# Kernel optimization log

Hardware: AMD Instinct MI355X
Metric: run time of the kernel (lower is better)

The kernel has to match this reference:

```python
import jax, jax.numpy as jnp
import numpy as np

NUM_HEADS = 16
HEAD_DIM = 64  # d_out // num_heads = 1024 // 16


def setup_inputs() -> dict:
    key = jax.random.key(0)
    ks = jax.random.split(key, 9)
    B, S, D = 2, 2048, 1024
    scale = 0.02
    return {
        "x": jax.random.normal(ks[0], (B, S, D), jnp.float32),
        "Wq": jax.random.normal(ks[1], (D, D), jnp.float32) * scale,
        "bq": jax.random.normal(ks[2], (D,), jnp.float32) * scale,
        "Wk": jax.random.normal(ks[3], (D, D), jnp.float32) * scale,
        "bk": jax.random.normal(ks[4], (D,), jnp.float32) * scale,
        "Wv": jax.random.normal(ks[5], (D, D), jnp.float32) * scale,
        "bv": jax.random.normal(ks[6], (D,), jnp.float32) * scale,
        "Wo": jax.random.normal(ks[7], (D, D), jnp.float32) * scale,
        "bo": jax.random.normal(ks[8], (D,), jnp.float32) * scale,
    }


def reference(x, Wq, bq, Wk, bk, Wv, bv, Wo, bo):
    B, S, D = x.shape
    H, Dh = NUM_HEADS, HEAD_DIM
    # QKV projections (torch Linear: x @ W.T + b; here W stored as [d_in, d_out])
    q = (x @ Wq + bq).reshape(B, S, H, Dh).transpose(0, 2, 1, 3)  # [B,H,S,Dh]
    k = (x @ Wk + bk).reshape(B, S, H, Dh).transpose(0, 2, 1, 3)
    v = (x @ Wv + bv).reshape(B, S, H, Dh).transpose(0, 2, 1, 3)
    scores = jnp.einsum("bhqd,bhkd->bhqk", q, k)
    # causal mask applied before scaling (as in source; -inf unaffected by scale)
    causal = jnp.tril(jnp.ones((S, S), dtype=bool))
    scores = jnp.where(causal, scores, -jnp.inf) / jnp.sqrt(jnp.float32(Dh))
    attn = jax.nn.softmax(scores, axis=-1)  # dropout=0.0 (eval)
    ctx = jnp.einsum("bhqk,bhkd->bhqd", attn, v)  # [B,H,S,Dh]
    ctx = ctx.transpose(0, 2, 1, 3).reshape(B, S, D)
    return ctx @ Wo + bo
```

## Files before the change

### kernel.cpp

```cpp
#include <hip/hip_runtime.h>
#include <math.h>


#define H_  16
#define DH_ 64
#define D_  1024
#define S_  2048
#define B_  2

typedef __attribute__((ext_vector_type(8))) short short8;
typedef __attribute__((ext_vector_type(4))) float f32x4;

#define QSCALE 0.18033688011112042f
#define DEFER_THR 11.5416f

__device__ __forceinline__ unsigned short f2bf(float f) {
    union { float f; unsigned int u; } v; v.f = f;
    unsigned int r = (v.u + 0x7fffu + ((v.u >> 16) & 1u)) >> 16;
    return (unsigned short)r;
}

__device__ __forceinline__ unsigned cvt_pk_bf16(float lo, float hi) {
    unsigned r;
    asm("v_cvt_pk_bf16_f32 %0, %1, %2" : "=v"(r) : "v"(lo), "v"(hi));
    return r;
}

__device__ __forceinline__ float fast_exp2(float x) {
#if __has_builtin(__builtin_amdgcn_exp2f)
    return __builtin_amdgcn_exp2f(x);
#else
    return exp2f(x);
#endif
}

__device__ __forceinline__ void gload_lds16(const void* g, void* l) {
    __builtin_amdgcn_global_load_lds(
        (const __attribute__((address_space(1))) void*)g,
        (__attribute__((address_space(3))) void*)l, 16, 0, 0);
}

#define SYNC_VM0() asm volatile("s_waitcnt vmcnt(0)\n\ts_barrier" ::: "memory")

__global__ __launch_bounds__(256) void cvt_x_k(const float* __restrict__ x,
                                               unsigned short* __restrict__ xb)
{
    int i = (blockIdx.x * 256 + threadIdx.x) * 8;
    float4 a = *(const float4*)&x[i];
    float4 b = *(const float4*)&x[i + 4];
    uint4 o;
    o.x = f2bf(a.x) | ((unsigned)f2bf(a.y) << 16);
    o.y = f2bf(a.z) | ((unsigned)f2bf(a.w) << 16);
    o.z = f2bf(b.x) | ((unsigned)f2bf(b.y) << 16);
    o.w = f2bf(b.z) | ((unsigned)f2bf(b.w) << 16);
    *(uint4*)&xb[i] = o;
}

__global__ __launch_bounds__(256) void tr_w_k(
    const float* __restrict__ W0, const float* __restrict__ W1,
    const float* __restrict__ W2, const float* __restrict__ W3,
    unsigned short* __restrict__ wt)
{
    const float* W = W0;
    if (blockIdx.z == 1) W = W1; else if (blockIdx.z == 2) W = W2;
    else if (blockIdx.z == 3) W = W3;
    unsigned short* out = wt + (size_t)blockIdx.z * 1048576;

    __shared__ float t[64][65];
    const int k0 = blockIdx.x * 64, n0 = blockIdx.y * 64;
    const int r = threadIdx.x >> 4, c4 = (threadIdx.x & 15) * 4;

    #pragma unroll
    for (int p = 0; p < 4; ++p) {
        float4 v = *(const float4*)&W[(size_t)(k0 + r + 16 * p) * D_ + n0 + c4];
        t[r + 16 * p][c4 + 0] = v.x; t[r + 16 * p][c4 + 1] = v.y;
        t[r + 16 * p][c4 + 2] = v.z; t[r + 16 * p][c4 + 3] = v.w;
    }
    __syncthreads();
    #pragma unroll
    for (int p = 0; p < 4; ++p) {
        int nn = r + 16 * p;
        uint2 o;
        o.x = f2bf(t[c4 + 0][nn]) | ((unsigned)f2bf(t[c4 + 1][nn]) << 16);
        o.y = f2bf(t[c4 + 2][nn]) | ((unsigned)f2bf(t[c4 + 3][nn]) << 16);
        *(uint2*)&out[(size_t)(n0 + nn) * D_ + k0 + c4] = o;
    }
}

template<int QKV>
__global__ __launch_bounds__(256) void gemm_bf16(
    const unsigned short* __restrict__ Ab,
    const unsigned short* __restrict__ Wt,
    const float* __restrict__ b0, const float* __restrict__ b1,
    const float* __restrict__ b2,
    void* __restrict__ o0, void* __restrict__ o1, void* __restrict__ o2)
{
    const unsigned short* W = Wt;
    const float* bias = b0;
    int z = 0;
    if (QKV) {
        z = blockIdx.z;
        W = Wt + (size_t)z * 1048576;
        if (z == 1) bias = b1; else if (z == 2) bias = b2;
    }
    const int n0 = blockIdx.x * 128, j0 = blockIdx.y * 128;
    const int tid = threadIdx.x;
    const int lane = tid & 63;
    const int wq = tid >> 6, wm = wq >> 1, wn = wq & 1;
    const int lr = lane & 15, lk = lane >> 4;

    __shared__ __align__(16) char smem[32768];

    f32x4 acc[4][4] = {};

    for (int k0 = 0; k0 < D_; k0 += 64) {
        __syncthreads();
        #pragma unroll
        for (int c = 0; c < 4; ++c) {
            int u = c * 256 + tid;
            int r = u >> 3, sp = u & 7, sl = sp ^ (r & 7);
            gload_lds16(&Ab[(size_t)(n0 + r) * D_ + k0 + sl * 8], &smem[u * 16]);
        }
        #pragma unroll
        for (int c = 0; c < 4; ++c) {
            int u = c * 256 + tid;
            int r = u >> 3, sp = u & 7, sl = sp ^ (r & 7);
            gload_lds16(&W[(size_t)(j0 + r) * D_ + k0 + sl * 8],
                        &smem[16384 + u * 16]);
        }
        __syncthreads();
        #pragma unroll
        for (int kc = 0; kc < 2; ++kc) {
            short8 a[4], b[4];
            #pragma unroll
            for (int m = 0; m < 4; ++m) {
                int row = wm * 64 + m * 16 + lr;
                int sp = (kc * 4 + lk) ^ (row & 7);
                a[m] = *(const short8*)&smem[row * 128 + sp * 16];
            }
            #pragma unroll
            for (int n = 0; n < 4; ++n) {
                int row = wn * 64 + n * 16 + lr;
                int sp = (kc * 4 + lk) ^ (row & 7);
                b[n] = *(const short8*)&smem[16384 + row * 128 + sp * 16];
            }
            #pragma unroll
            for (int m = 0; m < 4; ++m)
                #pragma unroll
                for (int n = 0; n < 4; ++n)
                    acc[m][n] = __builtin_amdgcn_mfma_f32_16x16x32_bf16(
                        a[m], b[n], acc[m][n], 0, 0, 0);
        }
    }

    float bn[4];
    #pragma unroll
    for (int n = 0; n < 4; ++n) bn[n] = bias[j0 + wn * 64 + n * 16 + lr];

    if (QKV) {
        __syncthreads();
        char* ep = smem + wq * 8192;
        const int head = (j0 + wn * 64) >> 6;
        const int row0 = n0 + wm * 64;
        const float sc = (z == 0) ? QSCALE : 1.0f;

        if (z < 2) {
            #pragma unroll
            for (int m = 0; m < 4; ++m)
                #pragma unroll
                for (int n = 0; n < 4; ++n) {
                    int col = n * 16 + lr;
                    #pragma unroll
                    for (int r = 0; r < 4; ++r) {
                        int row = m * 16 + lk * 4 + r;
                        int phys = (col >> 3) ^ (row & 7);
                        *(unsigned short*)&ep[row * 128 + phys * 16 + (col & 7) * 2]
                            = f2bf((acc[m][n][r] + bn[n]) * sc);
                    }
                }
            unsigned short* out = (unsigned short*)(z == 0 ? o0 : o1);
            #pragma unroll
            for (int p8 = 0; p8 < 8; ++p8) {
                int row = p8 * 8 + (lane >> 3);
                int phys = (lane & 7) ^ (row & 7);
                uint4 pk = *(const uint4*)&ep[row * 128 + phys * 16];
                int nrow = row0 + row;
                int bb = nrow >> 11, s = nrow & (S_ - 1);
                *(uint4*)&out[(((size_t)(bb * H_ + head)) * S_ + s) * 64
                              + (lane & 7) * 8] = pk;
            }
        } else {
            #pragma unroll
            for (int m = 0; m < 4; ++m)
                #pragma unroll
                for (int n = 0; n < 4; ++n) {
                    int row = n * 16 + lr;
                    #pragma unroll
                    for (int r = 0; r < 4; ++r) {
                        int col = m * 16 + lk * 4 + r;
                        int phys = (col >> 3) ^ (row & 7);
                        *(unsigned short*)&ep[row * 128 + phys * 16 + (col & 7) * 2]
                            = f2bf(acc[m][n][r] + bn[n]);
                    }
                }
            unsigned short* out = (unsigned short*)o2;
            int bb = row0 >> 11, s0 = row0 & (S_ - 1);
            #pragma unroll
            for (int p8 = 0; p8 < 8; ++p8) {
                int dh = p8 * 8 + (lane >> 3);
                int phys = (lane & 7) ^ (dh & 7);
                uint4 pk = *(const uint4*)&ep[dh * 128 + phys * 16];
                *(uint4*)&out[(((size_t)(bb * H_ + head)) * 64 + dh) * S_
                              + s0 + (lane & 7) * 8] = pk;
            }
        }
    } else {
        float* out = (float*)o0;
        #pragma unroll
        for (int m = 0; m < 4; ++m)
            #pragma unroll
            for (int n = 0; n < 4; ++n) {
                int col = j0 + wn * 64 + n * 16 + lr;
                int row0 = n0 + wm * 64 + m * 16 + lk * 4;
                #pragma unroll
                for (int r = 0; r < 4; ++r)
                    out[(size_t)(row0 + r) * D_ + col] = acc[m][n][r] + bn[n];
            }
    }
}

__global__ __launch_bounds__(256) void attn_mfma(
    const unsigned short* __restrict__ q, const unsigned short* __restrict__ k,
    const unsigned short* __restrict__ vt, unsigned short* __restrict__ ctx)
{
    const int bh = blockIdx.x;
    const int qt = 31 - blockIdx.y;
    const int tid = threadIdx.x;
    const int lane = tid & 63, wq = tid >> 6;
    const int lx = lane & 15, hi = lane >> 4;

    __shared__ __align__(16) char smem[40960];
    char* Pw = &smem[32768 + wq * 2048];

    const int b = bh >> 4, h = bh & (H_ - 1);

    short8 qf[2];
    {
        const unsigned short* qrow =
            q + ((size_t)bh * S_ + qt * 64 + wq * 16 + lx) * 64;
        qf[0] = *(const short8*)&qrow[hi * 8];
        qf[1] = *(const short8*)&qrow[32 + hi * 8];
    }

    f32x4 o[4] = {};
    float m = -INFINITY, l = 0.f;
    const int qg = qt * 64 + wq * 16 + lx;

    {
        #pragma unroll
        for (int c = 0; c < 2; ++c) {
            int u = c * 256 + tid;
            int r = u >> 3, sp = u & 7, sl = sp ^ (r & 7);
            gload_lds16(&k[((size_t)bh * S_ + r) * 64 + sl * 8], &smem[u * 16]);
        }
        #pragma unroll
        for (int c = 0; c < 2; ++c) {
            int u = c * 256 + tid;
            int r = u >> 3, sp = u & 7, sl = sp ^ (r & 7);
            gload_lds16(&vt[((size_t)bh * 64 + r) * S_ + sl * 8],
                        &smem[8192 + u * 16]);
        }
    }
    SYNC_VM0();

    int cur = 0;
    for (int kt = 0; kt <= qt; ++kt) {
        char* bufc = smem + cur * 16384;

        if (kt < qt) {
            char* bufn = smem + (cur ^ 1) * 16384;
            #pragma unroll
            for (int c = 0; c < 2; ++c) {
                int u = c * 256 + tid;
                int r = u >> 3, sp = u & 7, sl = sp ^ (r & 7);
                gload_lds16(&k[((size_t)bh * S_ + (kt + 1) * 64 + r) * 64 + sl * 8],
                            &bufn[u * 16]);
            }
            #pragma unroll
            for (int c = 0; c < 2; ++c) {
                int u = c * 256 + tid;
                int r = u >> 3, sp = u & 7, sl = sp ^ (r & 7);
                gload_lds16(&vt[((size_t)bh * 64 + r) * S_ + (kt + 1) * 64 + sl * 8],
                            &bufn[8192 + u * 16]);
            }
        }

        f32x4 s[4] = {};
        #pragma unroll
        for (int rt = 0; rt < 4; ++rt) {
            #pragma unroll
            for (int ks = 0; ks < 2; ++ks) {
                int row = rt * 16 + lx;
                int sp = (ks * 4 + hi) ^ (row & 7);
                short8 kf = *(const short8*)&bufc[row * 128 + sp * 16];
                s[rt] = __builtin_amdgcn_mfma_f32_16x16x32_bf16(
                    kf, qf[ks], s[rt], 0, 0, 0);
            }
        }

        if (kt == qt) {
            #pragma unroll
            for (int rt = 0; rt < 4; ++rt)
                #pragma unroll
                for (int r = 0; r < 4; ++r) {
                    int kvg = kt * 64 + rt * 16 + hi * 4 + r;
                    if (kvg > qg) s[rt][r] = -INFINITY;
                }
        }

        float tmax = s[0][0];
        #pragma unroll
        for (int rt = 0; rt < 4; ++rt)
            tmax = fmaxf(tmax, fmaxf(fmaxf(s[rt][0], s[rt][1]),
                                     fmaxf(s[rt][2], s[rt][3])));
        tmax = fmaxf(tmax, __shfl_xor(tmax, 16));
        tmax = fmaxf(tmax, __shfl_xor(tmax, 32));

        if (__any(tmax > m + DEFER_THR)) {
            float mn = fmaxf(m, tmax);
            float corr = fast_exp2(m - mn);
            m = mn;
            float ps = 0.f;
            #pragma unroll
            for (int rt = 0; rt < 4; ++rt)
                #pragma unroll
                for (int r = 0; r < 4; ++r) {
                    s[rt][r] = fast_exp2(s[rt][r] - mn);
                    ps += s[rt][r];
                }
            ps += __shfl_xor(ps, 16);
            ps += __shfl_xor(ps, 32);
            l = l * corr + ps;
            #pragma unroll
            for (int r = 0; r < 4; ++r) {
                float cr = __shfl(corr, hi * 4 + r);
                #pragma unroll
                for (int ct = 0; ct < 4; ++ct) o[ct][r] *= cr;
            }
        } else {
            float ps = 0.f;
            #pragma unroll
            for (int rt = 0; rt < 4; ++rt)
                #pragma unroll
                for (int r = 0; r < 4; ++r) {
                    s[rt][r] = fast_exp2(s[rt][r] - m);
                    ps += s[rt][r];
                }
            ps += __shfl_xor(ps, 16);
            ps += __shfl_xor(ps, 32);
            l += ps;
        }

        #pragma unroll
        for (int rt = 0; rt < 4; ++rt) {
            uint2 pk;
            pk.x = cvt_pk_bf16(s[rt][0], s[rt][1]);
            pk.y = cvt_pk_bf16(s[rt][2], s[rt][3]);
            int sl = 2 * rt + (hi >> 1);
            *(uint2*)&Pw[lx * 128 + ((sl ^ (lx & 7)) * 16) + (hi & 1) * 8] = pk;
        }
        short8 pf[2];
        #pragma unroll
        for (int ks = 0; ks < 2; ++ks) {
            int sl = ks * 4 + hi;
            pf[ks] = *(const short8*)&Pw[lx * 128 + ((sl ^ (lx & 7)) * 16)];
        }

        #pragma unroll
        for (int ct = 0; ct < 4; ++ct) {
            #pragma unroll
            for (int ks = 0; ks < 2; ++ks) {
                int row = ct * 16 + lx;
                int sp = (ks * 4 + hi) ^ (row & 7);
                short8 vf = *(const short8*)&bufc[8192 + row * 128 + sp * 16];
                o[ct] = __builtin_amdgcn_mfma_f32_16x16x32_bf16(
                    pf[ks], vf, o[ct], 0, 0, 0);
            }
        }

        SYNC_VM0();
        cur ^= 1;
    }

    #pragma unroll
    for (int r = 0; r < 4; ++r) {
        float inv = 1.0f / __shfl(l, hi * 4 + r);
        int srow = qt * 64 + wq * 16 + hi * 4 + r;
        #pragma unroll
        for (int ct = 0; ct < 4; ++ct)
            ctx[((size_t)(b * S_ + srow)) * D_ + h * 64 + ct * 16 + lx] =
                f2bf(o[ct][r] * inv);
    }
}

extern "C" void kernel_launch(void* const* d_in, const int* in_sizes, int n_in,
                              void* d_out, int out_size, void* d_ws, size_t ws_size,
                              hipStream_t stream)
{
    const float* x  = (const float*)d_in[0];
    const float* Wq = (const float*)d_in[1];
    const float* bq = (const float*)d_in[2];
    const float* Wk = (const float*)d_in[3];
    const float* bk = (const float*)d_in[4];
    const float* Wv = (const float*)d_in[5];
    const float* bv = (const float*)d_in[6];
    const float* Wo = (const float*)d_in[7];
    const float* bo = (const float*)d_in[8];
    float* out = (float*)d_out;

    const size_t per = (size_t)B_ * H_ * S_ * DH_;
    unsigned short* qb  = (unsigned short*)d_ws;
    unsigned short* kb  = qb + per;
    unsigned short* vtb = kb + per;
    unsigned short* xb  = vtb + per;
    unsigned short* wt  = xb + per;
    unsigned short* cb  = xb;

    cvt_x_k<<<2048, 256, 0, stream>>>(x, xb);
    tr_w_k<<<dim3(16, 16, 4), 256, 0, stream>>>(Wq, Wk, Wv, Wo, wt);

    gemm_bf16<1><<<dim3(32, 8, 3), 256, 0, stream>>>(
        xb, wt, bq, bk, bv, qb, kb, vtb);

    attn_mfma<<<dim3(32, 32), 256, 0, stream>>>(qb, kb, vtb, cb);

    gemm_bf16<0><<<dim3(32, 8, 1), 256, 0, stream>>>(
        cb, wt + 3u * 1048576u, bo, nullptr, nullptr, out, nullptr, nullptr);
}
```

Measured before the change: 197.5 us.

## Double query rows per attention block and write QKV epilogue directly

Each attention block now handles 128 query rows, with every wave computing two 16-row groups. This reuses each K/V tile loaded into LDS across twice as many queries and halves the grid. Block order is remapped so heavy and light causal tiles are interleaved. The QKV GEMM epilogue drops its LDS-staged, coalesced store path and writes straight to global with scattered 2-byte stores for Q/K and 8-byte stores for V^T. That removes a sync and LDS traffic but may hurt store coalescing. The attention change also raises register pressure and LDS use per block.

```diff
diff --git a/kernel.cpp b/kernel.cpp
--- a/kernel.cpp
+++ b/kernel.cpp
@@ -157,75 +157,39 @@
     #pragma unroll
     for (int n = 0; n < 4; ++n) bn[n] = bias[j0 + wn * 64 + n * 16 + lr];
 
-    if (QKV) {
-        __syncthreads();
-        char* ep = smem + wq * 8192;
-        const int head = (j0 + wn * 64) >> 6;
-        const int row0 = n0 + wm * 64;
-        const float sc = (z == 0) ? QSCALE : 1.0f;
-
-        if (z < 2) {
-            #pragma unroll
-            for (int m = 0; m < 4; ++m)
-                #pragma unroll
-                for (int n = 0; n < 4; ++n) {
-                    int col = n * 16 + lr;
-                    #pragma unroll
-                    for (int r = 0; r < 4; ++r) {
-                        int row = m * 16 + lk * 4 + r;
-                        int phys = (col >> 3) ^ (row & 7);
-                        *(unsigned short*)&ep[row * 128 + phys * 16 + (col & 7) * 2]
-                            = f2bf((acc[m][n][r] + bn[n]) * sc);
-                    }
+    #pragma unroll
+    for (int m = 0; m < 4; ++m) {
+        #pragma unroll
+        for (int n = 0; n < 4; ++n) {
+            int col = j0 + wn * 64 + n * 16 + lr;
+            int row0 = n0 + wm * 64 + m * 16 + lk * 4;
+            if (QKV) {
+                int head = col >> 6, dh = col & 63;
+                int bb = row0 >> 11, s0 = row0 & (S_ - 1);
+                float v0 = acc[m][n][0] + bn[n], v1 = acc[m][n][1] + bn[n];
+                float v2 = acc[m][n][2] + bn[n], v3 = acc[m][n][3] + bn[n];
+                if (z < 2) {
+                    const float sc = (z == 0) ? QSCALE : 1.0f;
+                    unsigned short* out = (unsigned short*)(z == 0 ? o0 : o1);
+                    size_t base = ((size_t)((bb << 4) + head) * S_) * 64 + dh;
+                    out[base + (size_t)(s0 + 0) * 64] = f2bf(v0 * sc);
+                    out[base + (size_t)(s0 + 1) * 64] = f2bf(v1 * sc);
+                    out[base + (size_t)(s0 + 2) * 64] = f2bf(v2 * sc);
+                    out[base + (size_t)(s0 + 3) * 64] = f2bf(v3 * sc);
+                } else {
+                    unsigned short* out = (unsigned short*)o2;
+                    uint2 pk;
+                    pk.x = f2bf(v0) | ((unsigned)f2bf(v1) << 16);
+                    pk.y = f2bf(v2) | ((unsigned)f2bf(v3) << 16);
+                    *(uint2*)&out[((size_t)((bb << 4) + head) * 64 + dh) * S_ + s0] = pk;
                 }
-            unsigned short* out = (unsigned short*)(z == 0 ? o0 : o1);
-            #pragma unroll
-            for (int p8 = 0; p8 < 8; ++p8) {
-                int row = p8 * 8 + (lane >> 3);
-                int phys = (lane & 7) ^ (row & 7);
-                uint4 pk = *(const uint4*)&ep[row * 128 + phys * 16];
-                int nrow = row0 + row;
-                int bb = nrow >> 11, s = nrow & (S_ - 1);
-                *(uint4*)&out[(((size_t)(bb * H_ + head)) * S_ + s) * 64
-                              + (lane & 7) * 8] = pk;
-            }
-        } else {
-            #pragma unroll
-            for (int m = 0; m < 4; ++m)
-                #pragma unroll
-                for (int n = 0; n < 4; ++n) {
-                    int row = n * 16 + lr;
-                    #pragma unroll
-                    for (int r = 0; r < 4; ++r) {
-                        int col = m * 16 + lk * 4 + r;
-                        int phys = (col >> 3) ^ (row & 7);
-                        *(unsigned short*)&ep[row * 128 + phys * 16 + (col & 7) * 2]
-                            = f2bf(acc[m][n][r] + bn[n]);
-                    }
-                }
-            unsigned short* out = (unsigned short*)o2;
-            int bb = row0 >> 11, s0 = row0 & (S_ - 1);
-            #pragma unroll
-            for (int p8 = 0; p8 < 8; ++p8) {
-                int dh = p8 * 8 + (lane >> 3);
-                int phys = (lane & 7) ^ (dh & 7);
-                uint4 pk = *(const uint4*)&ep[dh * 128 + phys * 16];
-                *(uint4*)&out[(((size_t)(bb * H_ + head)) * 64 + dh) * S_
-                              + s0 + (lane & 7) * 8] = pk;
-            }
-        }
-    } else {
-        float* out = (float*)o0;
-        #pragma unroll
-        for (int m = 0; m < 4; ++m)
-            #pragma unroll
-            for (int n = 0; n < 4; ++n) {
-                int col = j0 + wn * 64 + n * 16 + lr;
-                int row0 = n0 + wm * 64 + m * 16 + lk * 4;
+            } else {
+                float* out = (float*)o0;
                 #pragma unroll
                 for (int r = 0; r < 4; ++r)
                     out[(size_t)(row0 + r) * D_ + col] = acc[m][n][r] + bn[n];
             }
+        }
     }
 }
 
@@ -234,50 +198,53 @@
     const unsigned short* __restrict__ vt, unsigned short* __restrict__ ctx)
 {
     const int bh = blockIdx.x;
-    const int qt = 31 - blockIdx.y;
+    const int yt = blockIdx.y;
+    const int qt = (yt < 8) ? (15 - yt) : (yt - 8);
+    const int nkt = 2 * qt + 2;
     const int tid = threadIdx.x;
     const int lane = tid & 63, wq = tid >> 6;
     const int lx = lane & 15, hi = lane >> 4;
 
-    __shared__ __align__(16) char smem[40960];
-    char* Pw = &smem[32768 + wq * 2048];
+    __shared__ __align__(16) char smem[49152];
+    char* Pw0 = &smem[32768 + wq * 4096];
+    char* Pw1 = Pw0 + 2048;
 
     const int b = bh >> 4, h = bh & (H_ - 1);
 
-    short8 qf[2];
-    {
+    short8 qf[2][2];
+    #pragma unroll
+    for (int g = 0; g < 2; ++g) {
         const unsigned short* qrow =
-            q + ((size_t)bh * S_ + qt * 64 + wq * 16 + lx) * 64;
-        qf[0] = *(const short8*)&qrow[hi * 8];
-        qf[1] = *(const short8*)&qrow[32 + hi * 8];
-    }
-
-    f32x4 o[4] = {};
-    float m = -INFINITY, l = 0.f;
-    const int qg = qt * 64 + wq * 16 + lx;
-
-    {
-        #pragma unroll
-        for (int c = 0; c < 2; ++c) {
-            int u = c * 256 + tid;
-            int r = u >> 3, sp = u & 7, sl = sp ^ (r & 7);
-            gload_lds16(&k[((size_t)bh * S_ + r) * 64 + sl * 8], &smem[u * 16]);
-        }
-        #pragma unroll
-        for (int c = 0; c < 2; ++c) {
-            int u = c * 256 + tid;
-            int r = u >> 3, sp = u & 7, sl = sp ^ (r & 7);
-            gload_lds16(&vt[((size_t)bh * 64 + r) * S_ + sl * 8],
-                        &smem[8192 + u * 16]);
-        }
+            q + ((size_t)bh * S_ + qt * 128 + wq * 32 + g * 16 + lx) * 64;
+        qf[g][0] = *(const short8*)&qrow[hi * 8];
+        qf[g][1] = *(const short8*)&qrow[32 + hi * 8];
+    }
+
+    f32x4 o0[4] = {}, o1[4] = {};
+    float m0 = -INFINITY, m1 = -INFINITY, l0 = 0.f, l1 = 0.f;
+    const int qg0 = qt * 128 + wq * 32 + lx;
+    const int qg1 = qg0 + 16;
+
+    #pragma unroll
+    for (int c = 0; c < 2; ++c) {
+        int u = c * 256 + tid;
+        int r = u >> 3, sp = u & 7, sl = sp ^ (r & 7);
+        gload_lds16(&k[((size_t)bh * S_ + r) * 64 + sl * 8], &smem[u * 16]);
+    }
+    #pragma unroll
+    for (int c = 0; c < 2; ++c) {
+        int u = c * 256 + tid;
+        int r = u >> 3, sp = u & 7, sl = sp ^ (r & 7);
+        gload_lds16(&vt[((size_t)bh * 64 + r) * S_ + sl * 8],
+                    &smem[8192 + u * 16]);
     }
     SYNC_VM0();
 
     int cur = 0;
-    for (int kt = 0; kt <= qt; ++kt) {
+    for (int kt = 0; kt < nkt; ++kt) {
         char* bufc = smem + cur * 16384;
 
-        if (kt < qt) {
+        if (kt + 1 < nkt) {
             char* bufn = smem + (cur ^ 1) * 16384;
             #pragma unroll
             for (int c = 0; c < 2; ++c) {
@@ -295,7 +262,7 @@
             }
         }
 
-        f32x4 s[4] = {};
+        f32x4 s0[4] = {}, s1[4] = {};
         #pragma unroll
         for (int rt = 0; rt < 4; ++rt) {
             #pragma unroll
@@ -303,77 +270,91 @@
                 int row = rt * 16 + lx;
                 int sp = (ks * 4 + hi) ^ (row & 7);
                 short8 kf = *(const short8*)&bufc[row * 128 + sp * 16];
-                s[rt] = __builtin_amdgcn_mfma_f32_16x16x32_bf16(
-                    kf, qf[ks], s[rt], 0, 0, 0);
-            }
-        }
-
-        if (kt == qt) {
+                s0[rt] = __builtin_amdgcn_mfma_f32_16x16x32_bf16(
+                    kf, qf[0][ks], s0[rt], 0, 0, 0);
+                s1[rt] = __builtin_amdgcn_mfma_f32_16x16x32_bf16(
+                    kf, qf[1][ks], s1[rt], 0, 0, 0);
+            }
+        }
+
+        if (kt >= 2 * qt) {
             #pragma unroll
             for (int rt = 0; rt < 4; ++rt)
                 #pragma unroll
                 for (int r = 0; r < 4; ++r) {
                     int kvg = kt * 64 + rt * 16 + hi * 4 + r;
-                    if (kvg > qg) s[rt][r] = -INFINITY;
+                    if (kvg > qg0) s0[rt][r] = -INFINITY;
+                    if (kvg > qg1) s1[rt][r] = -INFINITY;
                 }
         }
 
-        float tmax = s[0][0];
-        #pragma unroll
-        for (int rt = 0; rt < 4; ++rt)
-            tmax = fmaxf(tmax, fmaxf(fmaxf(s[rt][0], s[rt][1]),
-                                     fmaxf(s[rt][2], s[rt][3])));
-        tmax = fmaxf(tmax, __shfl_xor(tmax, 16));
-        tmax = fmaxf(tmax, __shfl_xor(tmax, 32));
-
-        if (__any(tmax > m + DEFER_THR)) {
-            float mn = fmaxf(m, tmax);
-            float corr = fast_exp2(m - mn);
-            m = mn;
-            float ps = 0.f;
+        #pragma unroll
+        for (int g = 0; g < 2; ++g) {
+            f32x4* s = g ? s1 : s0;
+            float& m = g ? m1 : m0;
+            float& l = g ? l1 : l0;
+            f32x4* o = g ? o1 : o0;
+
+            float tmax = s[0][0];
             #pragma unroll
             for (int rt = 0; rt < 4; ++rt)
+                tmax = fmaxf(tmax, fmaxf(fmaxf(s[rt][0], s[rt][1]),
+                                         fmaxf(s[rt][2], s[rt][3])));
+            tmax = fmaxf(tmax, __shfl_xor(tmax, 16));
+            tmax = fmaxf(tmax, __shfl_xor(tmax, 32));
+
+            if (__any(tmax > m + DEFER_THR)) {
+                float mn = fmaxf(m, tmax);
+                float corr = fast_exp2(m - mn);
+                m = mn;
+                float ps = 0.f;
+                #pragma unroll
+                for (int rt = 0; rt < 4; ++rt)
+                    #pragma unroll
+                    for (int r = 0; r < 4; ++r) {
+                        s[rt][r] = fast_exp2(s[rt][r] - mn);
+                        ps += s[rt][r];
+                    }
+                ps += __shfl_xor(ps, 16);
+                ps += __shfl_xor(ps, 32);
+                l = l * corr + ps;
                 #pragma unroll
                 for (int r = 0; r < 4; ++r) {
-                    s[rt][r] = fast_exp2(s[rt][r] - mn);
-                    ps += s[rt][r];
+                    float cr = __shfl(corr, hi * 4 + r);
+                    #pragma unroll
+                    for (int ct = 0; ct < 4; ++ct) o[ct][r] *= cr;
                 }
-            ps += __shfl_xor(ps, 16);
-            ps += __shfl_xor(ps, 32);
-            l = l * corr + ps;
-            #pragma unroll
-            for (int r = 0; r < 4; ++r) {
-                float cr = __shfl(corr, hi * 4 + r);
-                #pragma unroll
-                for (int ct = 0; ct < 4; ++ct) o[ct][r] *= cr;
-            }
-        } else {
-            float ps = 0.f;
-            #pragma unroll
-            for (int rt = 0; rt < 4; ++rt)
-                #pragma unroll
-                for (int r = 0; r < 4; ++r) {
-                    s[rt][r] = fast_exp2(s[rt][r] - m);
-                    ps += s[rt][r];
-                }
-            ps += __shfl_xor(ps, 16);
-            ps += __shfl_xor(ps, 32);
-            l += ps;
-        }
-
-        #pragma unroll
-        for (int rt = 0; rt < 4; ++rt) {
-            uint2 pk;
-            pk.x = cvt_pk_bf16(s[rt][0], s[rt][1]);
-            pk.y = cvt_pk_bf16(s[rt][2], s[rt][3]);
-            int sl = 2 * rt + (hi >> 1);
-            *(uint2*)&Pw[lx * 128 + ((sl ^ (lx & 7)) * 16) + (hi & 1) * 8] = pk;
-        }
-        short8 pf[2];
+            } else {
+                float ps = 0.f;
+                #pragma unroll
+                for (int rt = 0; rt < 4; ++rt)
+                    #pragma unroll
+                    for (int r = 0; r < 4; ++r) {
+                        s[rt][r] = fast_exp2(s[rt][r] - m);
+                        ps += s[rt][r];
+                    }
+                ps += __shfl_xor(ps, 16);
+                ps += __shfl_xor(ps, 32);
+                l += ps;
+            }
+
+            char* Pw = g ? Pw1 : Pw0;
+            #pragma unroll
+            for (int rt = 0; rt < 4; ++rt) {
+                uint2 pk;
+                pk.x = cvt_pk_bf16(s[rt][0], s[rt][1]);
+                pk.y = cvt_pk_bf16(s[rt][2], s[rt][3]);
+                int sl = 2 * rt + (hi >> 1);
+                *(uint2*)&Pw[lx * 128 + ((sl ^ (lx & 7)) * 16) + (hi & 1) * 8] = pk;
+            }
+        }
+
+        short8 pf0[2], pf1[2];
         #pragma unroll
         for (int ks = 0; ks < 2; ++ks) {
             int sl = ks * 4 + hi;
-            pf[ks] = *(const short8*)&Pw[lx * 128 + ((sl ^ (lx & 7)) * 16)];
+            pf0[ks] = *(const short8*)&Pw0[lx * 128 + ((sl ^ (lx & 7)) * 16)];
+            pf1[ks] = *(const short8*)&Pw1[lx * 128 + ((sl ^ (lx & 7)) * 16)];
         }
 
         #pragma unroll
@@ -383,8 +364,10 @@
                 int row = ct * 16 + lx;
                 int sp = (ks * 4 + hi) ^ (row & 7);
                 short8 vf = *(const short8*)&bufc[8192 + row * 128 + sp * 16];
-                o[ct] = __builtin_amdgcn_mfma_f32_16x16x32_bf16(
-                    pf[ks], vf, o[ct], 0, 0, 0);
+                o0[ct] = __builtin_amdgcn_mfma_f32_16x16x32_bf16(
+                    pf0[ks], vf, o0[ct], 0, 0, 0);
+                o1[ct] = __builtin_amdgcn_mfma_f32_16x16x32_bf16(
+                    pf1[ks], vf, o1[ct], 0, 0, 0);
             }
         }
 
@@ -393,13 +376,18 @@
     }
 
     #pragma unroll
-    for (int r = 0; r < 4; ++r) {
-        float inv = 1.0f / __shfl(l, hi * 4 + r);
-        int srow = qt * 64 + wq * 16 + hi * 4 + r;
-        #pragma unroll
-        for (int ct = 0; ct < 4; ++ct)
-            ctx[((size_t)(b * S_ + srow)) * D_ + h * 64 + ct * 16 + lx] =
-                f2bf(o[ct][r] * inv);
+    for (int g = 0; g < 2; ++g) {
+        f32x4* o = g ? o1 : o0;
+        float lv = g ? l1 : l0;
+        #pragma unroll
+        for (int r = 0; r < 4; ++r) {
+            float inv = 1.0f / __shfl(lv, hi * 4 + r);
+            int srow = qt * 128 + wq * 32 + g * 16 + hi * 4 + r;
+            #pragma unroll
+            for (int ct = 0; ct < 4; ++ct)
+                ctx[((size_t)(b * S_ + srow)) * D_ + h * 64 + ct * 16 + lx] =
+                    f2bf(o[ct][r] * inv);
+        }
     }
 }
 
@@ -432,7 +420,7 @@
     gemm_bf16<1><<<dim3(32, 8, 3), 256, 0, stream>>>(
         xb, wt, bq, bk, bv, qb, kb, vtb);
 
-    attn_mfma<<<dim3(32, 32), 256, 0, stream>>>(qb, kb, vtb, cb);
+    attn_mfma<<<dim3(32, 16), 256, 0, stream>>>(qb, kb, vtb, cb);
 
     gemm_bf16<0><<<dim3(32, 8, 1), 256, 0, stream>>>(
         cb, wt + 3u * 1048576u, bo, nullptr, nullptr, out, nullptr, nullptr);
```

New measurement: 198.9 us. About the same (+0.7%).
